# Kernel optimization log

Measured on AMD Instinct MI355X. Metric: run time of the kernel, lower is better.

Reference implementation:

```python
import jax, jax.numpy as jnp
import numpy as np

N = 100000        # number of nodes
E = 1600000       # number of edges (avg degree 16)
D_IN = 512
D_OUT = 64


def setup_inputs() -> dict:
    key = jax.random.key(0)
    k1, k2, k3, k4, k5 = jax.random.split(key, 5)
    inputs = jax.random.normal(k1, (N, D_IN), dtype=jnp.float32)
    weight = jax.random.normal(k2, (D_IN, D_OUT), dtype=jnp.float32)
    adj_vals = jax.random.uniform(k3, (E,), dtype=jnp.float32)
    adj_rows = jax.random.randint(k4, (E,), 0, N, dtype=jnp.int32)
    adj_cols = jax.random.randint(k5, (E,), 0, N, dtype=jnp.int32)
    return {
        "inputs": inputs,
        "weight": weight,
        "adj_vals": adj_vals,
        "adj_rows": adj_rows,
        "adj_cols": adj_cols,
    }


def reference(inputs, weight, adj_vals, adj_rows, adj_cols):
    # Dense projection: [N, D_IN] @ [D_IN, D_OUT] -> [N, D_OUT]
    h = inputs @ weight
    # Sparse adjacency spmm (COO): out[r] += vals[e] * h[c] for edge e=(r,c)
    msgs = adj_vals[:, None] * h[adj_cols]            # [E, D_OUT]
    agg = jax.ops.segment_sum(msgs, adj_rows, num_segments=N)  # [N, D_OUT]
    # activation = relu
    return jax.nn.relu(agg)
```

## Files before the change

kernel.cpp:

```cpp
#include <hip/hip_runtime.h>
#include <hip/hip_bf16.h>

#define D_OUT 64
#define K_DIM 512
#define RPB 128
#define RPB_SHIFT 7
#define EPB 8192
#define GCAP 3072
#define RCAP 3072
#define CPAD 16
#define NBK 1024

using short8  = __attribute__((ext_vector_type(8))) short;
using floatx4 = __attribute__((ext_vector_type(4))) float;

__device__ inline unsigned short f32_to_bf16(float f) {
    __hip_bfloat16 b = __float2bfloat16(f);
    return *reinterpret_cast<unsigned short*>(&b);
}

__device__ inline unsigned int pk_bf16(float lo, float hi) {
    __hip_bfloat162 p = __float22bfloat162_rn(make_float2(lo, hi));
    return *reinterpret_cast<unsigned int*>(&p);
}

__device__ inline float bf16lo_f32(unsigned int g) {
    return __uint_as_float(g << 16);
}
__device__ inline float bf16hi_f32(unsigned int g) {
    return __uint_as_float(g & 0xFFFF0000u);
}

__global__ void wt_kernel(const float* __restrict__ W, unsigned short* __restrict__ wf,
                          int* __restrict__ cursor, int nbuck) {
    int i = blockIdx.x * blockDim.x + threadIdx.x;
    if (i < D_OUT * K_DIM) {
        int j    = i & 7;
        int lane = (i >> 3) & 63;
        int s    = (i >> 9) & 15;
        int nb   = i >> 13;
        int k  = s * 32 + (lane >> 4) * 8 + j;
        int nn = nb * 16 + (lane & 15);
        wf[i] = f32_to_bf16(W[k * D_OUT + nn]);
    }
    if (i < nbuck) cursor[i * CPAD] = i * GCAP;
}

__global__ __launch_bounds__(256, 4) void gemm_part_kernel(
    const float* __restrict__ A, const unsigned short* __restrict__ wf,
    unsigned short* __restrict__ H, int n,
    const int* __restrict__ rows, const int* __restrict__ cols,
    const float* __restrict__ vals, int* __restrict__ cursor,
    int2* __restrict__ keys, int E, int nbuck, int npart) {
    __shared__ int sm[2 * NBK];

    const int tid = threadIdx.x;

    if (blockIdx.x < npart) {
        int* cnt  = sm;
        int* offs = sm + NBK;
        const int blk = blockIdx.x;

        for (int b = tid; b < nbuck; b += 256) cnt[b] = 0;
        __syncthreads();

        const int base = blk * EPB;
#pragma unroll
        for (int i = 0; i < EPB / 256; i++) {
            int e = base + tid + i * 256;
            if (e < E) atomicAdd(&cnt[rows[e] >> RPB_SHIFT], 1);
        }
        __syncthreads();

        for (int b = tid; b < nbuck; b += 256) {
            int c = cnt[b];
            offs[b] = c ? atomicAdd(&cursor[b * CPAD], c) : 0;
        }
        __syncthreads();

#pragma unroll
        for (int i = 0; i < EPB / 256; i++) {
            int e = base + tid + i * 256;
            if (e < E) {
                int r = rows[e];
                int c = cols[e];
                float v = vals[e];
                int b = r >> RPB_SHIFT;
                int p = atomicAdd(&offs[b], 1);
                if (p < (b + 1) * GCAP)
                    keys[p] = make_int2(c | ((r & (RPB - 1)) << 17), __float_as_int(v));
            }
        }
        return;
    }

    const int gbk  = blockIdx.x - npart;
    const int wv   = tid >> 6;
    const int lane = tid & 63;
    const int ln   = lane & 15;
    const int quad = lane >> 4;
    const int row0 = gbk * 128 + wv * 16;
    const int row1 = row0 + 64;

    int a0 = row0 + ln; if (a0 >= n) a0 = n - 1;
    int a1 = row1 + ln; if (a1 >= n) a1 = n - 1;
    const float* Arow0 = A + (size_t)a0 * K_DIM;
    const float* Arow1 = A + (size_t)a1 * K_DIM;
    const unsigned short* wfl = wf + lane * 8;

    floatx4 accA0 = {0.f,0.f,0.f,0.f}, accA1 = {0.f,0.f,0.f,0.f};
    floatx4 accA2 = {0.f,0.f,0.f,0.f}, accA3 = {0.f,0.f,0.f,0.f};
    floatx4 accB0 = {0.f,0.f,0.f,0.f}, accB1 = {0.f,0.f,0.f,0.f};
    floatx4 accB2 = {0.f,0.f,0.f,0.f}, accB3 = {0.f,0.f,0.f,0.f};

    for (int h0 = 0; h0 < K_DIM; h0 += 128) {
        float4 t0[8], t1[8];
#pragma unroll
        for (int s = 0; s < 4; s++) {
            t0[2 * s]     = *reinterpret_cast<const float4*>(Arow0 + h0 + s * 32 + quad * 8);
            t0[2 * s + 1] = *reinterpret_cast<const float4*>(Arow0 + h0 + s * 32 + quad * 8 + 4);
            t1[2 * s]     = *reinterpret_cast<const float4*>(Arow1 + h0 + s * 32 + quad * 8);
            t1[2 * s + 1] = *reinterpret_cast<const float4*>(Arow1 + h0 + s * 32 + quad * 8 + 4);
        }
        short8 ab0[4], ab1[4];
#pragma unroll
        for (int s = 0; s < 4; s++) {
            float4 x0 = t0[2 * s], x1 = t0[2 * s + 1];
            int4 pk;
            pk.x = (int)pk_bf16(x0.x, x0.y);
            pk.y = (int)pk_bf16(x0.z, x0.w);
            pk.z = (int)pk_bf16(x1.x, x1.y);
            pk.w = (int)pk_bf16(x1.z, x1.w);
            ab0[s] = *reinterpret_cast<short8*>(&pk);
            float4 y0 = t1[2 * s], y1 = t1[2 * s + 1];
            int4 qk;
            qk.x = (int)pk_bf16(y0.x, y0.y);
            qk.y = (int)pk_bf16(y0.z, y0.w);
            qk.z = (int)pk_bf16(y1.x, y1.y);
            qk.w = (int)pk_bf16(y1.z, y1.w);
            ab1[s] = *reinterpret_cast<short8*>(&qk);
        }
#pragma unroll
        for (int s = 0; s < 4; s++) {
            const unsigned short* base = wfl + h0 * 16 + s * 512;
            short8 b0 = *reinterpret_cast<const short8*>(base);
            short8 b1 = *reinterpret_cast<const short8*>(base + 8192);
            short8 b2 = *reinterpret_cast<const short8*>(base + 16384);
            short8 b3 = *reinterpret_cast<const short8*>(base + 24576);
            accA0 = __builtin_amdgcn_mfma_f32_16x16x32_bf16(ab0[s], b0, accA0, 0, 0, 0);
            accA1 = __builtin_amdgcn_mfma_f32_16x16x32_bf16(ab0[s], b1, accA1, 0, 0, 0);
            accA2 = __builtin_amdgcn_mfma_f32_16x16x32_bf16(ab0[s], b2, accA2, 0, 0, 0);
            accA3 = __builtin_amdgcn_mfma_f32_16x16x32_bf16(ab0[s], b3, accA3, 0, 0, 0);
            accB0 = __builtin_amdgcn_mfma_f32_16x16x32_bf16(ab1[s], b0, accB0, 0, 0, 0);
            accB1 = __builtin_amdgcn_mfma_f32_16x16x32_bf16(ab1[s], b1, accB1, 0, 0, 0);
            accB2 = __builtin_amdgcn_mfma_f32_16x16x32_bf16(ab1[s], b2, accB2, 0, 0, 0);
            accB3 = __builtin_amdgcn_mfma_f32_16x16x32_bf16(ab1[s], b3, accB3, 0, 0, 0);
        }
    }

#pragma unroll
    for (int r = 0; r < 4; r++) {
        int gr = row0 + quad * 4 + r;
        if (gr < n) {
            unsigned short* Hr = H + (size_t)gr * D_OUT;
            Hr[ln]      = f32_to_bf16(accA0[r]);
            Hr[16 + ln] = f32_to_bf16(accA1[r]);
            Hr[32 + ln] = f32_to_bf16(accA2[r]);
            Hr[48 + ln] = f32_to_bf16(accA3[r]);
        }
    }
#pragma unroll
    for (int r = 0; r < 4; r++) {
        int gr = row1 + quad * 4 + r;
        if (gr < n) {
            unsigned short* Hr = H + (size_t)gr * D_OUT;
            Hr[ln]      = f32_to_bf16(accB0[r]);
            Hr[16 + ln] = f32_to_bf16(accB1[r]);
            Hr[32 + ln] = f32_to_bf16(accB2[r]);
            Hr[48 + ln] = f32_to_bf16(accB3[r]);
        }
    }
}

__global__ __launch_bounds__(512) void sort_agg_kernel(
    const unsigned short* __restrict__ h, const int2* __restrict__ keys,
    const int* __restrict__ cursor, float* __restrict__ out, int N) {
    __shared__ int2 rec[RCAP];
    __shared__ int cnt[RPB];
    __shared__ int excl[RPB];
    __shared__ int cur[RPB];
    __shared__ int wtot[2];

    const int tid  = threadIdx.x;
    const int lane = tid & 63;
    const int wv   = tid >> 6;
    const int q    = lane >> 4;
    const int li   = lane & 15;
    const int b    = blockIdx.x;

    const int start = b * GCAP;
    int m = cursor[b * CPAD] - start;
    if (m > GCAP) m = GCAP;

    if (tid < RPB) cnt[tid] = 0;
    __syncthreads();

    for (int i = tid; i < m; i += 512) {
        int rl = keys[start + i].x >> 17;
        atomicAdd(&cnt[rl], 1);
    }
    __syncthreads();

    int v = 0, x = 0;
    if (tid < RPB) {
        v = cnt[tid];
        x = v;
#pragma unroll
        for (int d = 1; d < 64; d <<= 1) {
            int y = __shfl_up(x, d, 64);
            if (lane >= d) x += y;
        }
        if (lane == 63) wtot[tid >> 6] = x;
    }
    __syncthreads();
    if (tid < RPB) {
        int base = (tid >= 64) ? wtot[0] : 0;
        int ex = base + x - v;
        excl[tid] = ex;
        cur[tid]  = ex;
    }
    __syncthreads();

    for (int i = tid; i < m; i += 512) {
        int2 kv = keys[start + i];
        int rl = kv.x >> 17;
        int p = atomicAdd(&cur[rl], 1);
        if (p < RCAP) rec[p] = kv;
    }
    __syncthreads();

    const int row0 = b * RPB;
    for (int rl = wv; rl < RPB; rl += 8) {
        int s = excl[rl];
        int e = cur[rl];
        float4 acc = {0.f, 0.f, 0.f, 0.f};
        int j = s;
        for (; j + 8 <= e; j += 8) {
            int2 kA = rec[j + q];
            int2 kB = rec[j + 4 + q];
            const uint2 gA = *reinterpret_cast<const uint2*>(
                h + (size_t)(kA.x & 0x1FFFF) * D_OUT + li * 4);
            const uint2 gB = *reinterpret_cast<const uint2*>(
                h + (size_t)(kB.x & 0x1FFFF) * D_OUT + li * 4);
            float vA = __int_as_float(kA.y);
            float vB = __int_as_float(kB.y);
            acc.x += vA * bf16lo_f32(gA.x);
            acc.y += vA * bf16hi_f32(gA.x);
            acc.z += vA * bf16lo_f32(gA.y);
            acc.w += vA * bf16hi_f32(gA.y);
            acc.x += vB * bf16lo_f32(gB.x);
            acc.y += vB * bf16hi_f32(gB.x);
            acc.z += vB * bf16lo_f32(gB.y);
            acc.w += vB * bf16hi_f32(gB.y);
        }
        for (; j < e; j += 4) {
            bool on = (j + q) < e;
            int2 kv = rec[on ? j + q : j];
            const uint2 g = *reinterpret_cast<const uint2*>(
                h + (size_t)(kv.x & 0x1FFFF) * D_OUT + li * 4);
            float vv = on ? __int_as_float(kv.y) : 0.f;
            acc.x += vv * bf16lo_f32(g.x);
            acc.y += vv * bf16hi_f32(g.x);
            acc.z += vv * bf16lo_f32(g.y);
            acc.w += vv * bf16hi_f32(g.y);
        }
        acc.x += __shfl_xor(acc.x, 16, 64);
        acc.y += __shfl_xor(acc.y, 16, 64);
        acc.z += __shfl_xor(acc.z, 16, 64);
        acc.w += __shfl_xor(acc.w, 16, 64);
        acc.x += __shfl_xor(acc.x, 32, 64);
        acc.y += __shfl_xor(acc.y, 32, 64);
        acc.z += __shfl_xor(acc.z, 32, 64);
        acc.w += __shfl_xor(acc.w, 32, 64);

        if (q == 0) {
            int gr = row0 + rl;
            if (gr < N) {
                float4 o;
                o.x = fmaxf(acc.x, 0.f);
                o.y = fmaxf(acc.y, 0.f);
                o.z = fmaxf(acc.z, 0.f);
                o.w = fmaxf(acc.w, 0.f);
                *reinterpret_cast<float4*>(out + (size_t)gr * D_OUT + li * 4) = o;
            }
        }
    }
}

extern "C" void kernel_launch(void* const* d_in, const int* in_sizes, int n_in,
                              void* d_out, int out_size, void* d_ws, size_t ws_size,
                              hipStream_t stream) {
    const float* A    = (const float*)d_in[0];
    const float* W    = (const float*)d_in[1];
    const float* vals = (const float*)d_in[2];
    const int*   rows = (const int*)d_in[3];
    const int*   cols = (const int*)d_in[4];
    float* out = (float*)d_out;

    const int N = out_size / D_OUT;
    const int E = in_sizes[2];
    const int nbuck = (N + RPB - 1) >> RPB_SHIFT;
    const int nb = (E + EPB - 1) / EPB;
    const int gb = (N + 127) / 128;

    char* ws = (char*)d_ws;
    unsigned short* h      = (unsigned short*)ws;
    int2*           keys   = (int2*)(ws + (size_t)N * D_OUT * 2);
    unsigned short* wf     = (unsigned short*)((char*)keys + (size_t)nbuck * GCAP * 8);
    int*            cursor = (int*)((char*)wf + (size_t)D_OUT * K_DIM * 2);

    wt_kernel<<<(D_OUT * K_DIM + 255) / 256, 256, 0, stream>>>(W, wf, cursor, nbuck);
    gemm_part_kernel<<<nb + gb, 256, 0, stream>>>(A, wf, h, N,
                                                  rows, cols, vals, cursor, keys,
                                                  E, nbuck, nb);
    sort_agg_kernel<<<nbuck, 512, 0, stream>>>(h, keys, cursor, out, N);
}
```

Baseline: 376.7 us.

## Stage A tile through LDS with coalesced row-contiguous loads in GEMM

The GEMM part now loads the fp32 input tile with coalesced accesses: each group of 16 threads reads 64 contiguous floats of a row. It converts them to bf16 into a padded shared-memory tile, and each wave then reads its MFMA A fragments from LDS. Before, each lane read strided 32-byte pieces directly from its own row. The goal is better global-memory coalescing for the dominant 200MB input stream, at the cost of two block barriers per 64-column chunk and less in-flight load depth (8 float4 per thread per chunk instead of 16 per 128).

```diff
diff --git a/kernel.cpp b/kernel.cpp
--- a/kernel.cpp
+++ b/kernel.cpp
@@ -10,6 +10,7 @@
 #define RCAP 3072
 #define CPAD 16
 #define NBK 1024
+#define LROW 72
 
 using short8  = __attribute__((ext_vector_type(8))) short;
 using floatx4 = __attribute__((ext_vector_type(4))) float;
@@ -52,13 +53,13 @@
     const int* __restrict__ rows, const int* __restrict__ cols,
     const float* __restrict__ vals, int* __restrict__ cursor,
     int2* __restrict__ keys, int E, int nbuck, int npart) {
-    __shared__ int sm[2 * NBK];
+    __shared__ __align__(16) unsigned short ats[128 * LROW];
 
     const int tid = threadIdx.x;
 
     if (blockIdx.x < npart) {
-        int* cnt  = sm;
-        int* offs = sm + NBK;
+        int* cnt  = (int*)ats;
+        int* offs = cnt + NBK;
         const int blk = blockIdx.x;
 
         for (int b = tid; b < nbuck; b += 256) cnt[b] = 0;
@@ -99,62 +100,59 @@
     const int lane = tid & 63;
     const int ln   = lane & 15;
     const int quad = lane >> 4;
-    const int row0 = gbk * 128 + wv * 16;
+    const int blkrow0 = gbk * 128;
+    const int row0 = blkrow0 + wv * 16;
     const int row1 = row0 + 64;
 
-    int a0 = row0 + ln; if (a0 >= n) a0 = n - 1;
-    int a1 = row1 + ln; if (a1 >= n) a1 = n - 1;
-    const float* Arow0 = A + (size_t)a0 * K_DIM;
-    const float* Arow1 = A + (size_t)a1 * K_DIM;
     const unsigned short* wfl = wf + lane * 8;
+
+    const int srow = tid >> 4;
+    const int sseg = tid & 15;
 
     floatx4 accA0 = {0.f,0.f,0.f,0.f}, accA1 = {0.f,0.f,0.f,0.f};
     floatx4 accA2 = {0.f,0.f,0.f,0.f}, accA3 = {0.f,0.f,0.f,0.f};
     floatx4 accB0 = {0.f,0.f,0.f,0.f}, accB1 = {0.f,0.f,0.f,0.f};
     floatx4 accB2 = {0.f,0.f,0.f,0.f}, accB3 = {0.f,0.f,0.f,0.f};
 
-    for (int h0 = 0; h0 < K_DIM; h0 += 128) {
-        float4 t0[8], t1[8];
-#pragma unroll
-        for (int s = 0; s < 4; s++) {
-            t0[2 * s]     = *reinterpret_cast<const float4*>(Arow0 + h0 + s * 32 + quad * 8);
-            t0[2 * s + 1] = *reinterpret_cast<const float4*>(Arow0 + h0 + s * 32 + quad * 8 + 4);
-            t1[2 * s]     = *reinterpret_cast<const float4*>(Arow1 + h0 + s * 32 + quad * 8);
-            t1[2 * s + 1] = *reinterpret_cast<const float4*>(Arow1 + h0 + s * 32 + quad * 8 + 4);
-        }
-        short8 ab0[4], ab1[4];
-#pragma unroll
-        for (int s = 0; s < 4; s++) {
-            float4 x0 = t0[2 * s], x1 = t0[2 * s + 1];
-            int4 pk;
-            pk.x = (int)pk_bf16(x0.x, x0.y);
-            pk.y = (int)pk_bf16(x0.z, x0.w);
-            pk.z = (int)pk_bf16(x1.x, x1.y);
-            pk.w = (int)pk_bf16(x1.z, x1.w);
-            ab0[s] = *reinterpret_cast<short8*>(&pk);
-            float4 y0 = t1[2 * s], y1 = t1[2 * s + 1];
-            int4 qk;
-            qk.x = (int)pk_bf16(y0.x, y0.y);
-            qk.y = (int)pk_bf16(y0.z, y0.w);
-            qk.z = (int)pk_bf16(y1.x, y1.y);
-            qk.w = (int)pk_bf16(y1.z, y1.w);
-            ab1[s] = *reinterpret_cast<short8*>(&qk);
-        }
-#pragma unroll
-        for (int s = 0; s < 4; s++) {
-            const unsigned short* base = wfl + h0 * 16 + s * 512;
-            short8 b0 = *reinterpret_cast<const short8*>(base);
-            short8 b1 = *reinterpret_cast<const short8*>(base + 8192);
-            short8 b2 = *reinterpret_cast<const short8*>(base + 16384);
-            short8 b3 = *reinterpret_cast<const short8*>(base + 24576);
-            accA0 = __builtin_amdgcn_mfma_f32_16x16x32_bf16(ab0[s], b0, accA0, 0, 0, 0);
-            accA1 = __builtin_amdgcn_mfma_f32_16x16x32_bf16(ab0[s], b1, accA1, 0, 0, 0);
-            accA2 = __builtin_amdgcn_mfma_f32_16x16x32_bf16(ab0[s], b2, accA2, 0, 0, 0);
-            accA3 = __builtin_amdgcn_mfma_f32_16x16x32_bf16(ab0[s], b3, accA3, 0, 0, 0);
-            accB0 = __builtin_amdgcn_mfma_f32_16x16x32_bf16(ab1[s], b0, accB0, 0, 0, 0);
-            accB1 = __builtin_amdgcn_mfma_f32_16x16x32_bf16(ab1[s], b1, accB1, 0, 0, 0);
-            accB2 = __builtin_amdgcn_mfma_f32_16x16x32_bf16(ab1[s], b2, accB2, 0, 0, 0);
-            accB3 = __builtin_amdgcn_mfma_f32_16x16x32_bf16(ab1[s], b3, accB3, 0, 0, 0);
+    for (int c = 0; c < 8; c++) {
+        float4 t[8];
+#pragma unroll
+        for (int i = 0; i < 8; i++) {
+            int r = i * 16 + srow;
+            int gr = blkrow0 + r; if (gr >= n) gr = n - 1;
+            t[i] = *reinterpret_cast<const float4*>(
+                A + (size_t)gr * K_DIM + c * 64 + sseg * 4);
+        }
+        __syncthreads();
+#pragma unroll
+        for (int i = 0; i < 8; i++) {
+            int r = i * 16 + srow;
+            uint2 w;
+            w.x = pk_bf16(t[i].x, t[i].y);
+            w.y = pk_bf16(t[i].z, t[i].w);
+            *reinterpret_cast<uint2*>(&ats[r * LROW + sseg * 4]) = w;
+        }
+        __syncthreads();
+
+#pragma unroll
+        for (int s = 0; s < 2; s++) {
+            short8 a0 = *reinterpret_cast<const short8*>(
+                &ats[(wv * 16 + ln) * LROW + s * 32 + quad * 8]);
+            short8 a1 = *reinterpret_cast<const short8*>(
+                &ats[(64 + wv * 16 + ln) * LROW + s * 32 + quad * 8]);
+            const unsigned short* bb = wfl + (c * 2 + s) * 512;
+            short8 b0 = *reinterpret_cast<const short8*>(bb);
+            short8 b1 = *reinterpret_cast<const short8*>(bb + 8192);
+            short8 b2 = *reinterpret_cast<const short8*>(bb + 16384);
+            short8 b3 = *reinterpret_cast<const short8*>(bb + 24576);
+            accA0 = __builtin_amdgcn_mfma_f32_16x16x32_bf16(a0, b0, accA0, 0, 0, 0);
+            accA1 = __builtin_amdgcn_mfma_f32_16x16x32_bf16(a0, b1, accA1, 0, 0, 0);
+            accA2 = __builtin_amdgcn_mfma_f32_16x16x32_bf16(a0, b2, accA2, 0, 0, 0);
+            accA3 = __builtin_amdgcn_mfma_f32_16x16x32_bf16(a0, b3, accA3, 0, 0, 0);
+            accB0 = __builtin_amdgcn_mfma_f32_16x16x32_bf16(a1, b0, accB0, 0, 0, 0);
+            accB1 = __builtin_amdgcn_mfma_f32_16x16x32_bf16(a1, b1, accB1, 0, 0, 0);
+            accB2 = __builtin_amdgcn_mfma_f32_16x16x32_bf16(a1, b2, accB2, 0, 0, 0);
+            accB3 = __builtin_amdgcn_mfma_f32_16x16x32_bf16(a1, b3, accB3, 0, 0, 0);
         }
     }
 
```

Measured after the change: 375.7 us. Within noise of the previous version (-0.3%).
